# Performance work log

Hardware: AMD Instinct MI355X
Metric: run time of the kernel (lower is better)

## Reference

```python
import jax, jax.numpy as jnp
import numpy as np

N = 131072      # num nodes
T = 16          # tile (block) size, tile_rows == tile_cols
BR = N // T     # block rows = 8192
K = 8           # nonzero blocks per block-row
IN_F, HID, NCLS = 128, 256, 64
LN_EPS = 1e-5


def setup_inputs() -> dict:
    key = jax.random.key(0)
    ks = jax.random.split(key, 8)
    features = jax.random.normal(ks[0], (N, IN_F), dtype=jnp.float32)
    block_vals = jax.random.uniform(ks[1], (BR, K, T, T), dtype=jnp.float32) / (K * T)
    block_cols = jax.random.randint(ks[2], (BR, K), 0, BR, dtype=jnp.int32)
    W0 = jax.random.normal(ks[3], (IN_F, HID), dtype=jnp.float32) / np.sqrt(IN_F)
    W1 = jax.random.normal(ks[4], (HID, HID), dtype=jnp.float32) / np.sqrt(HID)
    W2 = jax.random.normal(ks[5], (HID, NCLS), dtype=jnp.float32) / np.sqrt(HID)
    return {
        "features": features,
        "block_vals": block_vals,
        "W0": W0, "b0": jnp.zeros((HID,), jnp.float32),
        "W1": W1, "b1": jnp.zeros((HID,), jnp.float32),
        "W2": W2, "b2": jnp.zeros((NCLS,), jnp.float32),
        "g0": jnp.ones((HID,), jnp.float32), "beta0": jnp.zeros((HID,), jnp.float32),
        "g1": jnp.ones((HID,), jnp.float32), "beta1": jnp.zeros((HID,), jnp.float32),
        "block_cols": block_cols,
    }


def bcsr_spmm(block_vals, block_cols, z):
    """Block-CSR sparse matmul: out = A @ z.
    block_vals: [BR, K, T, T], block_cols: [BR, K] (block-column ids), z: [N, F]."""
    f = z.shape[-1]
    zb = z.reshape(BR, T, f)[block_cols]          # gather column blocks -> [BR, K, T, F]
    out = jnp.einsum('bkrc,bkcf->brf', block_vals, zb)  # block GEMM + accumulate over K
    return out.reshape(N, f)


def layer_norm(x, g, b):
    mu = jnp.mean(x, axis=-1, keepdims=True)
    var = jnp.mean(jnp.square(x - mu), axis=-1, keepdims=True)
    return g * (x - mu) * jax.lax.rsqrt(var + LN_EPS) + b


def reference(features, block_vals, W0, b0, W1, b1, W2, b2,
              g0, beta0, g1, beta1, block_cols):
    # layer 0: h' = A @ (h W0) + b0 ; relu ; LayerNorm
    h = bcsr_spmm(block_vals, block_cols, features @ W0) + b0
    h = layer_norm(jax.nn.relu(h), g0, beta0)
    # layer 1
    h = bcsr_spmm(block_vals, block_cols, h @ W1) + b1
    h = layer_norm(jax.nn.relu(h), g1, beta1)
    # output layer (no activation/norm)
    h = bcsr_spmm(block_vals, block_cols, h @ W2) + b2
    return h
```

## Files before the change

kernel.cpp:

```cpp
#include <hip/hip_runtime.h>
#include <hip/hip_bf16.h>


typedef __bf16 bf16;
typedef bf16 bf16x8 __attribute__((ext_vector_type(8)));
typedef bf16 bf16x4 __attribute__((ext_vector_type(4)));
typedef float f32x4 __attribute__((ext_vector_type(4)));

#define N_NODES 131072
#define BRQ 8192
#define KNZ 8
#define IN_F 128
#define HID 256
#define NCLS 64

static __device__ __forceinline__ f32x4 mfma16(bf16x8 a, bf16x8 b, f32x4 c) {
  return __builtin_amdgcn_mfma_f32_16x16x32_bf16(a, b, c, 0, 0, 0);
}

static __device__ __forceinline__ bf16x8 load8(const bf16* p) {
  return *(const bf16x8*)p;
}
static __device__ __forceinline__ bf16x8 cvt8(f32x4 a0, f32x4 a1) {
  bf16x8 r;
  r[0] = (bf16)a0[0]; r[1] = (bf16)a0[1]; r[2] = (bf16)a0[2]; r[3] = (bf16)a0[3];
  r[4] = (bf16)a1[0]; r[5] = (bf16)a1[1]; r[6] = (bf16)a1[2]; r[7] = (bf16)a1[3];
  return r;
}
static __device__ __forceinline__ bf16x8 load8(const float* p) {
  f32x4 a0 = *(const f32x4*)p;
  f32x4 a1 = *(const f32x4*)(p + 4);
  return cvt8(a0, a1);
}

template<typename TA, int KIN, int FOUT, int GRID>
static __device__ __forceinline__ void gemm_body(int wgid, int tid,
                                                 const TA* __restrict__ X,
                                                 const float* __restrict__ W,
                                                 bf16* __restrict__ Zbt) {
  constexpr int CG  = FOUT / 64;
  constexpr int KS  = KIN / 32;
  constexpr int RTS = GRID * 4 / CG;
  constexpr int NT  = BRQ / RTS;

  const int wave = tid >> 6;
  const int lane = tid & 63;
  const int l15  = lane & 15;
  const int quad = lane >> 4;
  const int gw   = wgid * 4 + wave;
  const int cg   = gw % CG;
  const int rt0  = gw / CG;

  bf16x8 wbf[KS][4];
#pragma unroll
  for (int k = 0; k < KS; ++k)
#pragma unroll
    for (int t = 0; t < 4; ++t) {
      const float* wp = W + (long)(k * 32 + quad * 8) * FOUT + cg * 64 + t * 16 + l15;
      bf16x8 v;
#pragma unroll
      for (int j = 0; j < 8; ++j) v[j] = (bf16)wp[(long)j * FOUT];
      wbf[k][t] = v;
    }

  const TA* __restrict__ xbase = X + (long)l15 * KIN + quad * 8;

  bf16x8 aw[2][KS];
#pragma unroll
  for (int k = 0; k < KS; ++k)
    aw[0][k] = load8(xbase + (long)rt0 * (16 * KIN) + k * 32);

#pragma unroll
  for (int it = 0; it < NT; ++it) {
    const int rt = rt0 + it * RTS;
    if (it + 1 < NT) {
      const long xoff = (long)(rt + RTS) * (16 * KIN);
#pragma unroll
      for (int k = 0; k < KS; ++k)
        aw[(it + 1) & 1][k] = load8(xbase + xoff + k * 32);
    }
    f32x4 acc[4] = {};
#pragma unroll
    for (int k = 0; k < KS; ++k)
#pragma unroll
      for (int t = 0; t < 4; ++t)
        acc[t] = mfma16(aw[it & 1][k], wbf[k][t], acc[t]);
#pragma unroll
    for (int t = 0; t < 4; ++t) {
      int col = cg * 64 + t * 16 + l15;
      bf16x4 v;
#pragma unroll
      for (int i = 0; i < 4; ++i) v[i] = (bf16)acc[t][i];
      *(bf16x4*)(Zbt + ((long)rt * FOUT + col) * 16 + quad * 4) = v;
    }
  }
}

__global__ __launch_bounds__(256) void gemm0_prep(const float* __restrict__ X,
                                                  const float* __restrict__ W,
                                                  bf16* __restrict__ Zbt,
                                                  const float* __restrict__ V,
                                                  bf16* __restrict__ Ab) {
  if (blockIdx.x < 1024) {
    gemm_body<float, IN_F, HID, 1024>(blockIdx.x, threadIdx.x, X, W, Zbt);
  } else {
    long i = ((long)(blockIdx.x - 1024) * 256 + threadIdx.x) * 8;
    f32x4 a0 = *(const f32x4*)(V + i);
    f32x4 a1 = *(const f32x4*)(V + i + 4);
    *(bf16x8*)(Ab + i) = cvt8(a0, a1);
  }
}

template<int KIN, int FOUT, int GRID>
__global__ __launch_bounds__(256) void gemm_bt2(const bf16* __restrict__ X,
                                                const float* __restrict__ W,
                                                bf16* __restrict__ Zbt) {
  gemm_body<bf16, KIN, FOUT, GRID>(blockIdx.x, threadIdx.x, X, W, Zbt);
}

__global__ __launch_bounds__(256) void spmm_ln(const bf16*  __restrict__ Abv,
                                               const int*   __restrict__ Abc,
                                               const bf16*  __restrict__ Zbt,
                                               const float* __restrict__ bias,
                                               const float* __restrict__ gamma,
                                               const float* __restrict__ beta,
                                               bf16* __restrict__ H) {
  const int wave = threadIdx.x >> 6;
  const int lane = threadIdx.x & 63;
  const int l15  = lane & 15;
  const int quad = lane >> 4;
  const int b    = blockIdx.x * 2 + (wave >> 1);
  const int ch   = wave & 1;

  const int*  bc    = Abc + b * KNZ;
  const int   cst   = (quad & 1) * 8;
  const int   half  = quad >> 1;
  const bf16* abase = Abv + (long)b * (KNZ * 256) + l15 * 16 + cst;

  bf16x8 afr[4];
  long   zb[4];
#pragma unroll
  for (int kp = 0; kp < 4; ++kp) {
    int blk = 2 * kp + half;
    afr[kp] = load8(abase + blk * 256);
    zb[kp]  = (long)bc[blk] * (HID * 16) + cst;
  }
  bf16x8 bfr[4][8];
#pragma unroll
  for (int kp = 0; kp < 4; ++kp)
#pragma unroll
    for (int t = 0; t < 8; ++t) {
      int f = ch * 128 + t * 16 + l15;
      bfr[kp][t] = *(const bf16x8*)(Zbt + zb[kp] + f * 16);
    }

  f32x4 acc[8] = {};
#pragma unroll
  for (int kp = 0; kp < 4; ++kp)
#pragma unroll
    for (int t = 0; t < 8; ++t)
      acc[t] = mfma16(afr[kp], bfr[kp][t], acc[t]);

  float gv[8], bv[8];
#pragma unroll
  for (int t = 0; t < 8; ++t) {
    int f = ch * 128 + t * 16 + l15;
    gv[t] = gamma[f];
    bv[t] = beta[f];
  }
  float ps[4] = {0.f, 0.f, 0.f, 0.f}, pss[4] = {0.f, 0.f, 0.f, 0.f};
#pragma unroll
  for (int t = 0; t < 8; ++t) {
    float bi = bias[ch * 128 + t * 16 + l15];
#pragma unroll
    for (int i = 0; i < 4; ++i) {
      float v = acc[t][i] + bi;
      v = v > 0.f ? v : 0.f;
      acc[t][i] = v;
      ps[i] += v;
      pss[i] += v * v;
    }
  }
#pragma unroll
  for (int m = 1; m < 16; m <<= 1) {
#pragma unroll
    for (int i = 0; i < 4; ++i) {
      ps[i]  += __shfl_xor(ps[i], m, 64);
      pss[i] += __shfl_xor(pss[i], m, 64);
    }
  }
  __shared__ float S[4][16], SS[4][16];
  if (l15 == 0) {
#pragma unroll
    for (int i = 0; i < 4; ++i) {
      S[wave][quad * 4 + i]  = ps[i];
      SS[wave][quad * 4 + i] = pss[i];
    }
  }
  __syncthreads();
#pragma unroll
  for (int i = 0; i < 4; ++i) {
    int r = quad * 4 + i;
    float s    = S[wave][r] + S[wave ^ 1][r];
    float ss   = SS[wave][r] + SS[wave ^ 1][r];
    float mu   = s * (1.f / 256.f);
    float var  = ss * (1.f / 256.f) - mu * mu;
    float rstd = rsqrtf(var + 1e-5f);
    bf16* hrow = H + (long)(b * 16 + r) * HID;
#pragma unroll
    for (int t = 0; t < 8; ++t) {
      int f = ch * 128 + t * 16 + l15;
      float y = (acc[t][i] - mu) * rstd * gv[t] + bv[t];
      hrow[f] = (bf16)y;
    }
  }
}

__global__ __launch_bounds__(256) void spmm_out(const bf16*  __restrict__ Abv,
                                                const int*   __restrict__ Abc,
                                                const bf16*  __restrict__ Zbt,
                                                const float* __restrict__ bias,
                                                float* __restrict__ out) {
  const int wave = threadIdx.x >> 6;
  const int b    = blockIdx.x * 4 + wave;
  const int lane = threadIdx.x & 63;
  const int l15  = lane & 15;
  const int quad = lane >> 4;

  const int*  bc    = Abc + b * KNZ;
  const int   cst   = (quad & 1) * 8;
  const int   half  = quad >> 1;
  const bf16* abase = Abv + (long)b * (KNZ * 256) + l15 * 16 + cst;

  bf16x8 afr[4];
  long   zb[4];
#pragma unroll
  for (int kp = 0; kp < 4; ++kp) {
    int blk = 2 * kp + half;
    afr[kp] = load8(abase + blk * 256);
    zb[kp]  = (long)bc[blk] * (NCLS * 16) + cst;
  }
  bf16x8 bfr[4][4];
#pragma unroll
  for (int kp = 0; kp < 4; ++kp)
#pragma unroll
    for (int t = 0; t < 4; ++t) {
      int f = t * 16 + l15;
      bfr[kp][t] = *(const bf16x8*)(Zbt + zb[kp] + f * 16);
    }

  f32x4 acc[4] = {};
#pragma unroll
  for (int kp = 0; kp < 4; ++kp)
#pragma unroll
    for (int t = 0; t < 4; ++t)
      acc[t] = mfma16(afr[kp], bfr[kp][t], acc[t]);

#pragma unroll
  for (int t = 0; t < 4; ++t) {
    int f = t * 16 + l15;
    float bi = bias[f];
#pragma unroll
    for (int i = 0; i < 4; ++i) {
      out[(long)(b * 16 + quad * 4 + i) * NCLS + f] = acc[t][i] + bi;
    }
  }
}

extern "C" void kernel_launch(void* const* d_in, const int* in_sizes, int n_in,
                              void* d_out, int out_size, void* d_ws, size_t ws_size,
                              hipStream_t stream) {
  const float* features = (const float*)d_in[0];
  const float* bvals    = (const float*)d_in[1];
  const float* W0       = (const float*)d_in[2];
  const float* b0v      = (const float*)d_in[3];
  const float* W1       = (const float*)d_in[4];
  const float* b1v      = (const float*)d_in[5];
  const float* W2       = (const float*)d_in[6];
  const float* b2v      = (const float*)d_in[7];
  const float* g0       = (const float*)d_in[8];
  const float* beta0    = (const float*)d_in[9];
  const float* g1       = (const float*)d_in[10];
  const float* beta1    = (const float*)d_in[11];
  const int*   bcols    = (const int*)d_in[12];
  float* outp = (float*)d_out;

  char* ws = (char*)d_ws;
  bf16* zbt0 = (bf16*)(ws + (64L << 20));
  bf16* h0   = (bf16*)ws;
  bf16* zbt1 = (bf16*)(ws + (64L << 20));
  bf16* h1   = (bf16*)ws;
  bf16* zbt2 = (bf16*)(ws + (64L << 20));

  bf16* Ab = (bf16*)d_out;

  gemm0_prep<<<dim3(1024 + BRQ), dim3(256), 0, stream>>>(features, W0, zbt0, bvals, Ab);
  spmm_ln<<<dim3(BRQ / 2), dim3(256), 0, stream>>>(Ab, bcols, zbt0, b0v, g0, beta0, h0);
  gemm_bt2<HID, HID, 1024><<<dim3(1024), dim3(256), 0, stream>>>(h0, W1, zbt1);
  spmm_ln<<<dim3(BRQ / 2), dim3(256), 0, stream>>>(Ab, bcols, zbt1, b1v, g1, beta1, h1);
  gemm_bt2<HID, NCLS, 512><<<dim3(512), dim3(256), 0, stream>>>(h1, W2, zbt2);
  spmm_out<<<dim3(BRQ / 4), dim3(256), 0, stream>>>(Ab, bcols, zbt2, b2v, outp);
}
```

Before: 490.3 us.

## Stage weights in LDS for dense GEMMs and read fp32 block values directly in SpMM

The dense GEMM kernels now load the weight column-group into shared memory once per workgroup, converting to bf16 and transposing with padding. MFMA B-fragments are read from LDS instead of being held in registers, which frees registers and allows occupancy 4. The separate fp32-to-bf16 conversion pass over the block values is removed, and the SpMM kernels read fp32 block values directly through the float load8 overload. In exchange, the SpMM kernels read twice the bytes for the A values each layer, and the GEMM gains LDS traffic plus a barrier.

```diff
diff --git a/kernel.cpp b/kernel.cpp
--- a/kernel.cpp
+++ b/kernel.cpp
@@ -34,34 +34,31 @@
 }
 
 template<typename TA, int KIN, int FOUT, int GRID>
-static __device__ __forceinline__ void gemm_body(int wgid, int tid,
-                                                 const TA* __restrict__ X,
-                                                 const float* __restrict__ W,
-                                                 bf16* __restrict__ Zbt) {
+__global__ __launch_bounds__(256, 4) void gemm_lds(const TA* __restrict__ X,
+                                                   const float* __restrict__ W,
+                                                   bf16* __restrict__ Zbt) {
   constexpr int CG  = FOUT / 64;
   constexpr int KS  = KIN / 32;
-  constexpr int RTS = GRID * 4 / CG;
+  constexpr int WGR = GRID / CG;
+  constexpr int RTS = WGR * 4;
   constexpr int NT  = BRQ / RTS;
-
+  constexpr int LDW = KIN + 8;
+
+  const int tid  = threadIdx.x;
   const int wave = tid >> 6;
   const int lane = tid & 63;
   const int l15  = lane & 15;
   const int quad = lane >> 4;
-  const int gw   = wgid * 4 + wave;
-  const int cg   = gw % CG;
-  const int rt0  = gw / CG;
-
-  bf16x8 wbf[KS][4];
-#pragma unroll
-  for (int k = 0; k < KS; ++k)
-#pragma unroll
-    for (int t = 0; t < 4; ++t) {
-      const float* wp = W + (long)(k * 32 + quad * 8) * FOUT + cg * 64 + t * 16 + l15;
-      bf16x8 v;
-#pragma unroll
-      for (int j = 0; j < 8; ++j) v[j] = (bf16)wp[(long)j * FOUT];
-      wbf[k][t] = v;
-    }
+  const int cg   = blockIdx.x % CG;
+  const int rg   = blockIdx.x / CG;
+  const int rt0  = rg * 4 + wave;
+
+  __shared__ bf16 WL[64 * LDW];
+
+  for (int e = tid; e < 64 * KIN; e += 256) {
+    int c = e & 63, k = e >> 6;
+    WL[c * LDW + k] = (bf16)W[(long)k * FOUT + cg * 64 + c];
+  }
 
   const TA* __restrict__ xbase = X + (long)l15 * KIN + quad * 8;
 
@@ -69,6 +66,8 @@
 #pragma unroll
   for (int k = 0; k < KS; ++k)
     aw[0][k] = load8(xbase + (long)rt0 * (16 * KIN) + k * 32);
+
+  __syncthreads();
 
 #pragma unroll
   for (int it = 0; it < NT; ++it) {
@@ -80,11 +79,16 @@
         aw[(it + 1) & 1][k] = load8(xbase + xoff + k * 32);
     }
     f32x4 acc[4] = {};
-#pragma unroll
-    for (int k = 0; k < KS; ++k)
-#pragma unroll
-      for (int t = 0; t < 4; ++t)
-        acc[t] = mfma16(aw[it & 1][k], wbf[k][t], acc[t]);
+    unsigned lo = 0;
+#pragma unroll
+    for (int k = 0; k < KS; ++k) {
+      asm volatile("" : "+v"(lo));
+#pragma unroll
+      for (int t = 0; t < 4; ++t) {
+        bf16x8 wf = *(const bf16x8*)(WL + lo + (t * 16 + l15) * LDW + k * 32 + quad * 8);
+        acc[t] = mfma16(aw[it & 1][k], wf, acc[t]);
+      }
+    }
 #pragma unroll
     for (int t = 0; t < 4; ++t) {
       int col = cg * 64 + t * 16 + l15;
@@ -96,29 +100,7 @@
   }
 }
 
-__global__ __launch_bounds__(256) void gemm0_prep(const float* __restrict__ X,
-                                                  const float* __restrict__ W,
-                                                  bf16* __restrict__ Zbt,
-                                                  const float* __restrict__ V,
-                                                  bf16* __restrict__ Ab) {
-  if (blockIdx.x < 1024) {
-    gemm_body<float, IN_F, HID, 1024>(blockIdx.x, threadIdx.x, X, W, Zbt);
-  } else {
-    long i = ((long)(blockIdx.x - 1024) * 256 + threadIdx.x) * 8;
-    f32x4 a0 = *(const f32x4*)(V + i);
-    f32x4 a1 = *(const f32x4*)(V + i + 4);
-    *(bf16x8*)(Ab + i) = cvt8(a0, a1);
-  }
-}
-
-template<int KIN, int FOUT, int GRID>
-__global__ __launch_bounds__(256) void gemm_bt2(const bf16* __restrict__ X,
-                                                const float* __restrict__ W,
-                                                bf16* __restrict__ Zbt) {
-  gemm_body<bf16, KIN, FOUT, GRID>(blockIdx.x, threadIdx.x, X, W, Zbt);
-}
-
-__global__ __launch_bounds__(256) void spmm_ln(const bf16*  __restrict__ Abv,
+__global__ __launch_bounds__(256) void spmm_ln(const float* __restrict__ Abv,
                                                const int*   __restrict__ Abc,
                                                const bf16*  __restrict__ Zbt,
                                                const float* __restrict__ bias,
@@ -132,10 +114,10 @@
   const int b    = blockIdx.x * 2 + (wave >> 1);
   const int ch   = wave & 1;
 
-  const int*  bc    = Abc + b * KNZ;
-  const int   cst   = (quad & 1) * 8;
-  const int   half  = quad >> 1;
-  const bf16* abase = Abv + (long)b * (KNZ * 256) + l15 * 16 + cst;
+  const int*   bc    = Abc + b * KNZ;
+  const int    cst   = (quad & 1) * 8;
+  const int    half  = quad >> 1;
+  const float* abase = Abv + (long)b * (KNZ * 256) + l15 * 16 + cst;
 
   bf16x8 afr[4];
   long   zb[4];
@@ -216,7 +198,7 @@
   }
 }
 
-__global__ __launch_bounds__(256) void spmm_out(const bf16*  __restrict__ Abv,
+__global__ __launch_bounds__(256) void spmm_out(const float* __restrict__ Abv,
                                                 const int*   __restrict__ Abc,
                                                 const bf16*  __restrict__ Zbt,
                                                 const float* __restrict__ bias,
@@ -227,10 +209,10 @@
   const int l15  = lane & 15;
   const int quad = lane >> 4;
 
-  const int*  bc    = Abc + b * KNZ;
-  const int   cst   = (quad & 1) * 8;
-  const int   half  = quad >> 1;
-  const bf16* abase = Abv + (long)b * (KNZ * 256) + l15 * 16 + cst;
+  const int*   bc    = Abc + b * KNZ;
+  const int    cst   = (quad & 1) * 8;
+  const int    half  = quad >> 1;
+  const float* abase = Abv + (long)b * (KNZ * 256) + l15 * 16 + cst;
 
   bf16x8 afr[4];
   long   zb[4];
@@ -292,12 +274,10 @@
   bf16* h1   = (bf16*)ws;
   bf16* zbt2 = (bf16*)(ws + (64L << 20));
 
-  bf16* Ab = (bf16*)d_out;
-
-  gemm0_prep<<<dim3(1024 + BRQ), dim3(256), 0, stream>>>(features, W0, zbt0, bvals, Ab);
-  spmm_ln<<<dim3(BRQ / 2), dim3(256), 0, stream>>>(Ab, bcols, zbt0, b0v, g0, beta0, h0);
-  gemm_bt2<HID, HID, 1024><<<dim3(1024), dim3(256), 0, stream>>>(h0, W1, zbt1);
-  spmm_ln<<<dim3(BRQ / 2), dim3(256), 0, stream>>>(Ab, bcols, zbt1, b1v, g1, beta1, h1);
-  gemm_bt2<HID, NCLS, 512><<<dim3(512), dim3(256), 0, stream>>>(h1, W2, zbt2);
-  spmm_out<<<dim3(BRQ / 4), dim3(256), 0, stream>>>(Ab, bcols, zbt2, b2v, outp);
-}
+  gemm_lds<float, IN_F, HID, 1024><<<dim3(1024), dim3(256), 0, stream>>>(features, W0, zbt0);
+  spmm_ln<<<dim3(BRQ / 2), dim3(256), 0, stream>>>(bvals, bcols, zbt0, b0v, g0, beta0, h0);
+  gemm_lds<bf16, HID, HID, 1024><<<dim3(1024), dim3(256), 0, stream>>>(h0, W1, zbt1);
+  spmm_ln<<<dim3(BRQ / 2), dim3(256), 0, stream>>>(bvals, bcols, zbt1, b1v, g1, beta1, h1);
+  gemm_lds<bf16, HID, NCLS, 512><<<dim3(512), dim3(256), 0, stream>>>(h1, W2, zbt2);
+  spmm_out<<<dim3(BRQ / 4), dim3(256), 0, stream>>>(bvals, bcols, zbt2, b2v, outp);
+}
```

After: 445.9 us (median of 2 runs). -9.0%, faster.
